# Optimization experiments

Measured on AMD Instinct MI355X. Metric: run time of the kernel, lower is better.

## Reference

```python
import jax, jax.numpy as jnp
import numpy as np

NUM_CLUSTERS = 5000  # labels.max()+1, fixed statically for jit
B, K, D, N = 256, 64, 2048, 50000
NHID, H2, NCLASS = 512, 256, 2


def setup_inputs() -> dict:
    key = jax.random.key(0)
    ks = jax.random.split(key, 16)
    s = lambda f_in: 1.0 / np.sqrt(f_in)
    return {
        "indexes": jax.random.randint(ks[0], (B,), 0, N),
        "features": jax.random.normal(ks[1], (N, D), dtype=jnp.float32),
        "labels": jax.random.randint(ks[2], (N,), 0, NUM_CLUSTERS),
        "domain": 1,
        "ori_0": 0,
        "ori_knn_neighbor": jax.random.randint(ks[3], (B, K), 0, N),
        "all_pred": jax.random.normal(ks[4], (B, K, NCLASS), dtype=jnp.float32),
        # GraphConv params (L-GCN style: weight [2*in, out])
        "W1": jax.random.normal(ks[5], (2 * D, NHID), jnp.float32) * s(2 * D),
        "b1": jnp.zeros((NHID,), jnp.float32),
        "W2": jax.random.normal(ks[6], (2 * NHID, H2), jnp.float32) * s(2 * NHID),
        "b2": jnp.zeros((H2,), jnp.float32),
        # classifier: Linear(256,256) -> PReLU(256) -> Linear(256,2)
        "Wc1": jax.random.normal(ks[7], (H2, H2), jnp.float32) * s(H2),
        "bc1": jnp.zeros((H2,), jnp.float32),
        "prelu_a": jnp.full((H2,), 0.25, jnp.float32),
        "Wc2": jax.random.normal(ks[8], (H2, NCLASS), jnp.float32) * s(H2),
        "bc2": jnp.zeros((NCLASS,), jnp.float32),
    }


def _gconv(x, A, W, b):
    # MeanAggregator: bmm(A, x); GraphConv: relu(cat([x, Ax]) @ W + b)
    agg = jnp.einsum('bkj,bjd->bkd', A, x)
    cat = jnp.concatenate([x, agg], axis=-1)
    return jax.nn.relu(jnp.einsum('bkd,df->bkf', cat, W) + b)


def reference(indexes, features, labels, domain, ori_0, ori_knn_neighbor, all_pred,
              W1, b1, W2, b2, Wc1, bc1, prelu_a, Wc2, bc2):
    # ---- cluster mean features (torch: index_add_ then divide; no_grad) ----
    clu_sum = jax.ops.segment_sum(features, labels, num_segments=NUM_CLUSTERS)
    nums = jax.ops.segment_sum(jnp.ones((features.shape[0],), features.dtype),
                               labels, num_segments=NUM_CLUSTERS)
    clu_mean = clu_sum / jnp.maximum(nums, 1.0)[:, None]  # [C, D]

    # ---- batched per-query subgraph construction (vectorized over B) ----
    clu_lab = labels[ori_knn_neighbor]            # [B, K]
    clu_feat = clu_mean[clu_lab]                  # [B, K, D]
    clu_feat = clu_feat.at[:, 0, :].set(features[indexes])  # pivot = raw feature

    A = jnp.einsum('bkd,bjd->bkj', clu_feat, clu_feat)       # pairwise similarity
    A = A * jnp.exp(all_pred[:, :, 1])[:, None, :]           # confidence weighting
    A = jax.nn.softmax(A, axis=-1)                           # row-normalized adjacency

    x = clu_feat / jnp.linalg.norm(clu_feat, axis=-1, keepdims=True)
    x = x - x[:, 0:1, :]                                     # center on pivot

    # (entire construction above is under torch.no_grad)
    x = jax.lax.stop_gradient(x)
    A = jax.lax.stop_gradient(A)

    # ---- GCN layers + classifier ----
    x = _gconv(x, A, W1, b1)      # [B, K, 512]
    x = _gconv(x, A, W2, b2)      # [B, K, 256]
    x0 = x.reshape(-1, H2)        # [B*K, 256]
    h = x0 @ Wc1 + bc1
    h = jnp.where(h >= 0, h, prelu_a * h)  # PReLU(256)
    logits = h @ Wc2 + bc2                 # [B*K, 2]

    # output_feat=True branch
    simm = jnp.sum(clu_mean * clu_mean, axis=1)                   # [C]
    pred = jax.nn.softmax(logits.reshape(B, K, NCLASS), axis=2)   # [B, K, 2]
    return (pred, simm)
```

## Files before the change

kernel.cpp:

```cpp
#include <hip/hip_runtime.h>
#include <math.h>

#define Bq 256
#define Kn 64
#define Dd 2048
#define Nn 50000
#define Cc 5000
#define NHID 512
#define H2d 256
#define LDH 264

typedef __attribute__((ext_vector_type(8))) __bf16 bf16x8;
typedef __attribute__((ext_vector_type(4))) float f32x4;

__device__ __forceinline__ unsigned short f2bf(float f) {
    union { float f; unsigned int u; } v;
    v.f = f;
    unsigned int u = v.u;
    unsigned int r = (u + 0x7fff + ((u >> 16) & 1)) >> 16;
    return (unsigned short)r;
}
__device__ __forceinline__ float bf2f(unsigned short h) {
    union { unsigned int u; float f; } v;
    v.u = ((unsigned int)h) << 16;
    return v.f;
}


__global__ void k_zero_int(int* __restrict__ p, int n) {
    int i = blockIdx.x * 256 + threadIdx.x;
    if (i < n) p[i] = 0;
}

__global__ void k_count(const int* __restrict__ labels, int* __restrict__ cnt, int n) {
    int i = blockIdx.x * 256 + threadIdx.x;
    if (i < n) atomicAdd(&cnt[labels[i]], 1);
}

__global__ __launch_bounds__(1024) void k_scan(const int* __restrict__ cnt,
                                               int* __restrict__ off,
                                               int* __restrict__ pos, int C) {
    __shared__ int s[1024];
    __shared__ int carry;
    int tid = threadIdx.x;
    if (tid == 0) carry = 0;
    __syncthreads();
    for (int base = 0; base < C; base += 1024) {
        int i = base + tid;
        int v = (i < C) ? cnt[i] : 0;
        s[tid] = v;
        __syncthreads();
        for (int o = 1; o < 1024; o <<= 1) {
            int t = (tid >= o) ? s[tid - o] : 0;
            __syncthreads();
            s[tid] += t;
            __syncthreads();
        }
        int excl = carry + s[tid] - v;
        if (i < C) { off[i] = excl; pos[i] = excl; }
        __syncthreads();
        if (tid == 0) carry += s[1023];
        __syncthreads();
    }
}

__global__ void k_scatter(const int* __restrict__ labels, int* __restrict__ pos,
                          int* __restrict__ rowidx, int n) {
    int i = blockIdx.x * 256 + threadIdx.x;
    if (i < n) {
        int p = atomicAdd(&pos[labels[i]], 1);
        rowidx[p] = i;
    }
}

__global__ __launch_bounds__(256) void k_meansimm(
    const float* __restrict__ feat, const int* __restrict__ rowidx,
    const int* __restrict__ off, const int* __restrict__ cnt,
    float* __restrict__ clu_mean, float* __restrict__ simm) {
    int c = blockIdx.x;
    int t = threadIdx.x;
    int n = cnt[c], st = off[c];
    float4 a0 = {0.f, 0.f, 0.f, 0.f}, a1 = {0.f, 0.f, 0.f, 0.f};
    for (int r = 0; r < n; r++) {
        const float* row = feat + (size_t)rowidx[st + r] * Dd;
        float4 v0 = *(const float4*)(row + t * 4);
        float4 v1 = *(const float4*)(row + 1024 + t * 4);
        a0.x += v0.x; a0.y += v0.y; a0.z += v0.z; a0.w += v0.w;
        a1.x += v1.x; a1.y += v1.y; a1.z += v1.z; a1.w += v1.w;
    }
    float sc = 1.f / (float)(n > 1 ? n : 1);
    a0.x *= sc; a0.y *= sc; a0.z *= sc; a0.w *= sc;
    a1.x *= sc; a1.y *= sc; a1.z *= sc; a1.w *= sc;
    float* outr = clu_mean + (size_t)c * Dd;
    *(float4*)(outr + t * 4) = a0;
    *(float4*)(outr + 1024 + t * 4) = a1;
    float ss = a0.x * a0.x + a0.y * a0.y + a0.z * a0.z + a0.w * a0.w +
               a1.x * a1.x + a1.y * a1.y + a1.z * a1.z + a1.w * a1.w;
    __shared__ float red[256];
    red[t] = ss;
    __syncthreads();
    for (int s2 = 128; s2 > 0; s2 >>= 1) {
        if (t < s2) red[t] += red[t + s2];
        __syncthreads();
    }
    if (t == 0) simm[c] = red[0];
}

__global__ __launch_bounds__(256) void k_build_ax(
    const float* __restrict__ feat, const float* __restrict__ clu_mean,
    const int* __restrict__ labels, const int* __restrict__ indexes,
    const int* __restrict__ knn, const float* __restrict__ all_pred,
    float* __restrict__ Abuf, unsigned short* __restrict__ xbuf) {
    __shared__ unsigned short Hs[64 * LDH];
    __shared__ unsigned short Ls[64 * LDH];
    __shared__ float Gs[64 * 65];
    __shared__ const float* rowp[64];
    __shared__ float wj64[64], rn[64];
    __shared__ float piv[2048];

    int b = blockIdx.x, tid = threadIdx.x;
    int wave = tid >> 6, lane = tid & 63, quad = lane >> 4, l16 = lane & 15;

    if (tid < 64) {
        const float* p = (tid == 0) ? feat + (size_t)indexes[b] * Dd
                                    : clu_mean + (size_t)labels[knn[b * 64 + tid]] * Dd;
        rowp[tid] = p;
        wj64[tid] = expf(all_pred[(b * 64 + tid) * 2 + 1]);
    }
    __syncthreads();

    f32x4 acc[4];
#pragma unroll
    for (int j = 0; j < 4; j++) acc[j] = (f32x4){0.f, 0.f, 0.f, 0.f};

    for (int ch = 0; ch < 8; ch++) {
        int d0 = ch * 256;
        __syncthreads();
#pragma unroll
        for (int q = 0; q < 16; q++) {
            int e4 = tid + q * 256;
            int row = e4 >> 6;
            int c4 = (e4 & 63) * 4;
            float4 v = *(const float4*)(rowp[row] + d0 + c4);
            ushort4 h, l;
            h.x = f2bf(v.x); l.x = f2bf(v.x - bf2f(h.x));
            h.y = f2bf(v.y); l.y = f2bf(v.y - bf2f(h.y));
            h.z = f2bf(v.z); l.z = f2bf(v.z - bf2f(h.z));
            h.w = f2bf(v.w); l.w = f2bf(v.w - bf2f(h.w));
            *(ushort4*)&Hs[row * LDH + c4] = h;
            *(ushort4*)&Ls[row * LDH + c4] = l;
        }
        __syncthreads();
#pragma unroll
        for (int ks = 0; ks < 8; ks++) {
            int kk = ks * 32 + quad * 8;
            bf16x8 ah = *(const bf16x8*)&Hs[(wave * 16 + l16) * LDH + kk];
            bf16x8 al = *(const bf16x8*)&Ls[(wave * 16 + l16) * LDH + kk];
#pragma unroll
            for (int j = 0; j < 4; j++) {
                bf16x8 bh = *(const bf16x8*)&Hs[(j * 16 + l16) * LDH + kk];
                bf16x8 bl = *(const bf16x8*)&Ls[(j * 16 + l16) * LDH + kk];
                acc[j] = __builtin_amdgcn_mfma_f32_16x16x32_bf16(ah, bh, acc[j], 0, 0, 0);
                acc[j] = __builtin_amdgcn_mfma_f32_16x16x32_bf16(ah, bl, acc[j], 0, 0, 0);
                acc[j] = __builtin_amdgcn_mfma_f32_16x16x32_bf16(al, bh, acc[j], 0, 0, 0);
            }
        }
    }
    __syncthreads();
#pragma unroll
    for (int j = 0; j < 4; j++)
#pragma unroll
        for (int r = 0; r < 4; r++)
            Gs[(wave * 16 + quad * 4 + r) * 65 + j * 16 + l16] = acc[j][r];
    __syncthreads();
    if (tid < 64) rn[tid] = rsqrtf(Gs[tid * 65 + tid]);
    __syncthreads();
    if (tid < 64) {
        int r = tid;
        float mx = -1e30f;
        for (int c = 0; c < 64; c++) {
            float v = Gs[r * 65 + c] * wj64[c];
            mx = fmaxf(mx, v);
        }
        float s = 0.f;
        for (int c = 0; c < 64; c++) {
            float e = expf(Gs[r * 65 + c] * wj64[c] - mx);
            Gs[r * 65 + c] = e;
            s += e;
        }
        float inv = 1.f / s;
        float* Arow = Abuf + ((size_t)b * 64 + r) * 64;
        for (int c = 0; c < 64; c++) Arow[c] = Gs[r * 65 + c] * inv;
    }
    __syncthreads();
    float rn0 = rn[0];
    const float* pivp = rowp[0];
    for (int c4 = tid; c4 < 512; c4 += 256) {
        float4 v = *(const float4*)(pivp + c4 * 4);
        v.x *= rn0; v.y *= rn0; v.z *= rn0; v.w *= rn0;
        *(float4*)&piv[c4 * 4] = v;
    }
    __syncthreads();
    unsigned short* xo = xbuf + (size_t)b * 64 * Dd;
    for (int e4 = tid; e4 < 64 * 512; e4 += 256) {
        int row = e4 >> 9;
        int c4 = (e4 & 511) * 4;
        float4 v = *(const float4*)(rowp[row] + c4);
        float r_ = rn[row];
        float4 p = *(const float4*)&piv[c4];
        ushort4 o_;
        o_.x = f2bf(v.x * r_ - p.x);
        o_.y = f2bf(v.y * r_ - p.y);
        o_.z = f2bf(v.z * r_ - p.z);
        o_.w = f2bf(v.w * r_ - p.w);
        *(ushort4*)&xo[row * Dd + c4] = o_;
    }
}

template <int SPLIT>
__global__ __launch_bounds__(256) void k_pack_w(const float* __restrict__ W,
                                                unsigned short* __restrict__ Bp,
                                                int K, int Nhalf) {
    int Ntot = SPLIT ? 2 * Nhalf : Nhalf;
    int idx = blockIdx.x * 256 + threadIdx.x;
    int kb = idx / Ntot;
    int n = idx - kb * Ntot;
    ushort4 lo, hi;
    float v[8];
#pragma unroll
    for (int j = 0; j < 8; j++) {
        int k = kb * 8 + j;
        if (SPLIT)
            v[j] = (n < Nhalf) ? W[(size_t)k * Nhalf + n]
                               : W[(size_t)(K + k) * Nhalf + (n - Nhalf)];
        else
            v[j] = W[(size_t)k * Nhalf + n];
    }
    lo.x = f2bf(v[0]); lo.y = f2bf(v[1]); lo.z = f2bf(v[2]); lo.w = f2bf(v[3]);
    hi.x = f2bf(v[4]); hi.y = f2bf(v[5]); hi.z = f2bf(v[6]); hi.w = f2bf(v[7]);
    *(ushort4*)&Bp[(size_t)idx * 8] = lo;
    *(ushort4*)&Bp[(size_t)idx * 8 + 4] = hi;
}

template <int EPI>
__global__ __launch_bounds__(256) void gemm_bf16_mfma(
    const unsigned short* __restrict__ A, const unsigned short* __restrict__ Bp,
    float* __restrict__ C, int M, int K, int N,
    const float* __restrict__ bias, const float* __restrict__ pre_a) {
    __shared__ unsigned short Asm[128 * 32];
    __shared__ unsigned short Bsm[4 * 128 * 8];
    int tid = threadIdx.x;
    int wave = tid >> 6, lane = tid & 63;
    int quad = lane >> 4, l16 = lane & 15;
    int m0 = blockIdx.y * 128, n0 = blockIdx.x * 128;
    int wm = (wave >> 1) * 64, wn = (wave & 1) * 64;

    f32x4 acc[4][4];
#pragma unroll
    for (int i = 0; i < 4; i++)
#pragma unroll
        for (int j = 0; j < 4; j++) acc[i][j] = (f32x4){0.f, 0.f, 0.f, 0.f};

    int ia0 = wave * 2, ia1 = wave * 2 + 1;
    const unsigned short* gA0 = A + (size_t)(m0 + ia0 * 16 + (lane >> 2)) * K + (lane & 3) * 8;
    const unsigned short* gA1 = gA0 + (size_t)16 * K;
    const unsigned short* gB0 = Bp + (size_t)(n0 + lane) * 8 + (size_t)wave * N * 8;

    for (int k0 = 0; k0 < K; k0 += 32) {
        __syncthreads();
        size_t bko = (size_t)(k0 >> 3) * N * 8;
        __builtin_amdgcn_global_load_lds(
            (const __attribute__((address_space(1))) void*)(gA0 + k0),
            (__attribute__((address_space(3))) void*)(Asm + ia0 * 512), 16, 0, 0);
        __builtin_amdgcn_global_load_lds(
            (const __attribute__((address_space(1))) void*)(gA1 + k0),
            (__attribute__((address_space(3))) void*)(Asm + ia1 * 512), 16, 0, 0);
        __builtin_amdgcn_global_load_lds(
            (const __attribute__((address_space(1))) void*)(gB0 + bko),
            (__attribute__((address_space(3))) void*)(Bsm + wave * 1024), 16, 0, 0);
        __builtin_amdgcn_global_load_lds(
            (const __attribute__((address_space(1))) void*)(gB0 + bko + 512),
            (__attribute__((address_space(3))) void*)(Bsm + wave * 1024 + 512), 16, 0, 0);
        __syncthreads();

        bf16x8 a[4], b[4];
#pragma unroll
        for (int i = 0; i < 4; i++)
            a[i] = *(const bf16x8*)&Asm[(wm + i * 16 + l16) * 32 + quad * 8];
#pragma unroll
        for (int j = 0; j < 4; j++)
            b[j] = *(const bf16x8*)&Bsm[quad * 1024 + (wn + j * 16 + l16) * 8];
#pragma unroll
        for (int i = 0; i < 4; i++)
#pragma unroll
            for (int j = 0; j < 4; j++)
                acc[i][j] = __builtin_amdgcn_mfma_f32_16x16x32_bf16(
                    a[i], b[j], acc[i][j], 0, 0, 0);
    }

#pragma unroll
    for (int i = 0; i < 4; i++) {
#pragma unroll
        for (int j = 0; j < 4; j++) {
            int col = n0 + wn + j * 16 + l16;
            float bcol = (EPI == 1) ? bias[col] : 0.f;
            float acol = (EPI == 1) ? pre_a[col] : 0.f;
#pragma unroll
            for (int r = 0; r < 4; r++) {
                int row = m0 + wm + i * 16 + quad * 4 + r;
                float v = acc[i][j][r];
                if (EPI == 1) {
                    v += bcol;
                    v = (v >= 0.f) ? v : acol * v;
                }
                C[(size_t)row * N + col] = v;
            }
        }
    }
}

template <int OBF>
__global__ __launch_bounds__(256) void k_layer_agg(
    const float* __restrict__ Uab, const float* __restrict__ Abuf,
    const float* __restrict__ bias, void* __restrict__ outp, int Nc) {
    int b = blockIdx.x;
    int tid = threadIdx.x;
    __shared__ float Ast[64 * 68];
    __shared__ float Us[64 * 68];
    int ty = tid >> 4, tx = tid & 15;
    const float* Ab = Abuf + (size_t)b * 64 * 64;
    for (int e4 = tid; e4 < 1024; e4 += 256) {
        float4 v = *(const float4*)(Ab + e4 * 4);
        int row = e4 >> 4;
        int c4 = (e4 & 15) * 4;
        Ast[(c4 + 0) * 68 + row] = v.x;
        Ast[(c4 + 1) * 68 + row] = v.y;
        Ast[(c4 + 2) * 68 + row] = v.z;
        Ast[(c4 + 3) * 68 + row] = v.w;
    }
    int ldU = 2 * Nc;
    const float* Ua = Uab;
    const float* Ub = Uab + Nc;
    for (int n0 = 0; n0 < Nc; n0 += 64) {
        __syncthreads();
#pragma unroll
        for (int kq = 0; kq < 4; kq++) {
            int e4 = tid + kq * 256;
            int row = e4 >> 4;
            int c4 = (e4 & 15) * 4;
            float4 v = *(const float4*)(Ub + (size_t)(b * 64 + row) * ldU + n0 + c4);
            *(float4*)&Us[row * 68 + c4] = v;
        }
        __syncthreads();
        float acc[4][4];
#pragma unroll
        for (int i = 0; i < 4; i++)
#pragma unroll
            for (int j = 0; j < 4; j++) acc[i][j] = 0.f;
        for (int kk = 0; kk < 64; kk++) {
            float4 a4 = *(const float4*)&Ast[kk * 68 + ty * 4];
            float4 b4 = *(const float4*)&Us[kk * 68 + tx * 4];
            float aa[4] = {a4.x, a4.y, a4.z, a4.w};
            float bb[4] = {b4.x, b4.y, b4.z, b4.w};
#pragma unroll
            for (int i = 0; i < 4; i++)
#pragma unroll
                for (int j = 0; j < 4; j++) acc[i][j] += aa[i] * bb[j];
        }
#pragma unroll
        for (int i = 0; i < 4; i++) {
            int m = b * 64 + ty * 4 + i;
            int n = n0 + tx * 4;
            float4 ua = *(const float4*)(Ua + (size_t)m * ldU + n);
            float v0 = fmaxf(ua.x + acc[i][0] + bias[n + 0], 0.f);
            float v1 = fmaxf(ua.y + acc[i][1] + bias[n + 1], 0.f);
            float v2 = fmaxf(ua.z + acc[i][2] + bias[n + 2], 0.f);
            float v3 = fmaxf(ua.w + acc[i][3] + bias[n + 3], 0.f);
            if (OBF) {
                ushort4 o_;
                o_.x = f2bf(v0); o_.y = f2bf(v1); o_.z = f2bf(v2); o_.w = f2bf(v3);
                *(ushort4*)((unsigned short*)outp + (size_t)m * Nc + n) = o_;
            } else {
                float4 o_ = {v0, v1, v2, v3};
                *(float4*)((float*)outp + (size_t)m * Nc + n) = o_;
            }
        }
        __syncthreads();
    }
}

__global__ __launch_bounds__(256) void k_logits(
    const float* __restrict__ h, const float* __restrict__ Wc2,
    const float* __restrict__ bc2, float* __restrict__ pred) {
    __shared__ float p0[256], p1[256];
    int tid = threadIdx.x;
    int r = tid >> 2, s = tid & 3;
    int m = blockIdx.x * 64 + r;
    const float* hr = h + (size_t)m * 256;
    float l0 = 0.f, l1 = 0.f;
    for (int k = s; k < 256; k += 4) {
        float hv = hr[k];
        l0 += hv * Wc2[2 * k];
        l1 += hv * Wc2[2 * k + 1];
    }
    p0[tid] = l0;
    p1[tid] = l1;
    __syncthreads();
    if (s == 0) {
        float L0 = p0[tid] + p0[tid + 1] + p0[tid + 2] + p0[tid + 3] + bc2[0];
        float L1 = p1[tid] + p1[tid + 1] + p1[tid + 2] + p1[tid + 3] + bc2[1];
        float mx = fmaxf(L0, L1);
        float e0 = expf(L0 - mx), e1 = expf(L1 - mx);
        float inv = 1.f / (e0 + e1);
        pred[2 * m] = e0 * inv;
        pred[2 * m + 1] = e1 * inv;
    }
}

extern "C" void kernel_launch(void* const* d_in, const int* in_sizes, int n_in,
                              void* d_out, int out_size, void* d_ws, size_t ws_size,
                              hipStream_t stream) {
    const int* indexes = (const int*)d_in[0];
    const float* features = (const float*)d_in[1];
    const int* labels = (const int*)d_in[2];
    const int* knn = (const int*)d_in[5];
    const float* all_pred = (const float*)d_in[6];
    const float* W1 = (const float*)d_in[7];
    const float* b1 = (const float*)d_in[8];
    const float* W2 = (const float*)d_in[9];
    const float* b2 = (const float*)d_in[10];
    const float* Wc1 = (const float*)d_in[11];
    const float* bc1 = (const float*)d_in[12];
    const float* pre_a = (const float*)d_in[13];
    const float* Wc2 = (const float*)d_in[14];
    const float* bc2 = (const float*)d_in[15];
    float* out = (float*)d_out;

    char* w = (char*)d_ws;
    size_t o = 0;
    auto carve = [&](size_t bytes) -> char* {
        char* p = w + o;
        o += (bytes + 255) & ~(size_t)255;
        return p;
    };
    int* cnt = (int*)carve((size_t)Cc * 4);
    int* off = (int*)carve((size_t)Cc * 4);
    int* pos = (int*)carve((size_t)Cc * 4);
    int* rowidx = (int*)carve((size_t)Nn * 4);
    float* clu_mean = (float*)carve((size_t)Cc * Dd * 4);
    unsigned short* xbuf = (unsigned short*)carve((size_t)Bq * Kn * Dd * 2);
    float* Abuf = (float*)carve((size_t)Bq * Kn * Kn * 4);
    float* U = (float*)carve((size_t)Bq * Kn * 2 * NHID * 4);
    unsigned short* Bp1 = (unsigned short*)carve((size_t)(Dd / 8) * 1024 * 8 * 2);
    unsigned short* x1 = (unsigned short*)carve((size_t)Bq * Kn * NHID * 2);
    float* V = (float*)carve((size_t)Bq * Kn * 2 * H2d * 4);
    unsigned short* Bp2 = (unsigned short*)carve((size_t)(NHID / 8) * 512 * 8 * 2);
    unsigned short* x2 = (unsigned short*)carve((size_t)Bq * Kn * H2d * 2);
    float* h = (float*)carve((size_t)Bq * Kn * H2d * 4);
    unsigned short* Bpc = (unsigned short*)carve((size_t)(H2d / 8) * 256 * 8 * 2);

    float* simm_out = out + (size_t)Bq * Kn * 2;

    k_zero_int<<<(Cc + 255) / 256, 256, 0, stream>>>(cnt, Cc);
    k_count<<<(Nn + 255) / 256, 256, 0, stream>>>(labels, cnt, Nn);
    k_scan<<<1, 1024, 0, stream>>>(cnt, off, pos, Cc);
    k_scatter<<<(Nn + 255) / 256, 256, 0, stream>>>(labels, pos, rowidx, Nn);

    k_meansimm<<<Cc, 256, 0, stream>>>(features, rowidx, off, cnt, clu_mean, simm_out);

    k_build_ax<<<Bq, 256, 0, stream>>>(features, clu_mean, labels, indexes, knn,
                                       all_pred, Abuf, xbuf);

    k_pack_w<1><<<(Dd / 8) * 1024 / 256, 256, 0, stream>>>(W1, Bp1, Dd, NHID);
    k_pack_w<1><<<(NHID / 8) * 512 / 256, 256, 0, stream>>>(W2, Bp2, NHID, H2d);
    k_pack_w<0><<<(H2d / 8) * 256 / 256, 256, 0, stream>>>(Wc1, Bpc, H2d, H2d);

    {
        dim3 g(1024 / 128, (Bq * Kn) / 128);
        gemm_bf16_mfma<0><<<g, 256, 0, stream>>>(xbuf, Bp1, U, Bq * Kn, Dd, 1024,
                                                 nullptr, nullptr);
    }
    k_layer_agg<1><<<Bq, 256, 0, stream>>>(U, Abuf, b1, x1, NHID);

    {
        dim3 g(512 / 128, (Bq * Kn) / 128);
        gemm_bf16_mfma<0><<<g, 256, 0, stream>>>(x1, Bp2, V, Bq * Kn, NHID, 512,
                                                 nullptr, nullptr);
    }
    k_layer_agg<1><<<Bq, 256, 0, stream>>>(V, Abuf, b2, x2, H2d);

    {
        dim3 g(256 / 128, (Bq * Kn) / 128);
        gemm_bf16_mfma<1><<<g, 256, 0, stream>>>(x2, Bpc, h, Bq * Kn, H2d, 256,
                                                 bc1, pre_a);
    }
    k_logits<<<(Bq * Kn) / 64, 256, 0, stream>>>(h, Wc2, bc2, out);

    (void)in_sizes; (void)n_in; (void)out_size; (void)ws_size;
}
```

Before: 906.7 us.

## Project unique cluster means through W1 once instead of per-neighbor rows

The first GCN layer's input rows are now built from a table of normalized cluster means plus normalized pivot rows (5376 rows in total). The first projection GEMM runs on that table instead of on 16384 materialized B*K rows, and the subtraction of the pivot is moved after the projection by linearity. A new aggregation kernel gathers the projected rows by label and subtracts the pivot's projection before the A-aggregation and ReLU. This removes the 64MB xbuf write and cuts the big GEMM's M dimension roughly threefold. In exchange it adds a pivot kernel, a padding zero-fill, gathered reads in the aggregation, and a slightly different rounding order (bf16 applied before the subtraction).

Measured after the change: 837.4 us. 1.08x faster.

```diff
diff --git a/kernel.cpp b/kernel.cpp
--- a/kernel.cpp
+++ b/kernel.cpp
@@ -9,6 +9,8 @@
 #define NHID 512
 #define H2d 256
 #define LDH 264
+#define MP 5376
+#define PIVROW 5120
 
 typedef __attribute__((ext_vector_type(8))) __bf16 bf16x8;
 typedef __attribute__((ext_vector_type(4))) float f32x4;
@@ -76,7 +78,8 @@
 __global__ __launch_bounds__(256) void k_meansimm(
     const float* __restrict__ feat, const int* __restrict__ rowidx,
     const int* __restrict__ off, const int* __restrict__ cnt,
-    float* __restrict__ clu_mean, float* __restrict__ simm) {
+    float* __restrict__ clu_mean, float* __restrict__ simm,
+    unsigned short* __restrict__ cn) {
     int c = blockIdx.x;
     int t = threadIdx.x;
     int n = cnt[c], st = off[c];
@@ -104,19 +107,56 @@
         __syncthreads();
     }
     if (t == 0) simm[c] = red[0];
+    float tot = red[0];
+    float rnn = (tot > 0.f) ? rsqrtf(tot) : 0.f;
+    ushort4 c0, c1;
+    c0.x = f2bf(a0.x * rnn); c0.y = f2bf(a0.y * rnn);
+    c0.z = f2bf(a0.z * rnn); c0.w = f2bf(a0.w * rnn);
+    c1.x = f2bf(a1.x * rnn); c1.y = f2bf(a1.y * rnn);
+    c1.z = f2bf(a1.z * rnn); c1.w = f2bf(a1.w * rnn);
+    unsigned short* cr = cn + (size_t)c * Dd;
+    *(ushort4*)(cr + t * 4) = c0;
+    *(ushort4*)(cr + 1024 + t * 4) = c1;
+}
+
+__global__ __launch_bounds__(256) void k_pivots(
+    const float* __restrict__ feat, const int* __restrict__ indexes,
+    unsigned short* __restrict__ PA) {
+    int b = blockIdx.x, t = threadIdx.x;
+    const float* row = feat + (size_t)indexes[b] * Dd;
+    float4 v0 = *(const float4*)(row + t * 4);
+    float4 v1 = *(const float4*)(row + 1024 + t * 4);
+    float ss = v0.x * v0.x + v0.y * v0.y + v0.z * v0.z + v0.w * v0.w +
+               v1.x * v1.x + v1.y * v1.y + v1.z * v1.z + v1.w * v1.w;
+    __shared__ float red[256];
+    red[t] = ss;
+    __syncthreads();
+    for (int s2 = 128; s2 > 0; s2 >>= 1) {
+        if (t < s2) red[t] += red[t + s2];
+        __syncthreads();
+    }
+    float tot = red[0];
+    float rnn = (tot > 0.f) ? rsqrtf(tot) : 0.f;
+    ushort4 c0, c1;
+    c0.x = f2bf(v0.x * rnn); c0.y = f2bf(v0.y * rnn);
+    c0.z = f2bf(v0.z * rnn); c0.w = f2bf(v0.w * rnn);
+    c1.x = f2bf(v1.x * rnn); c1.y = f2bf(v1.y * rnn);
+    c1.z = f2bf(v1.z * rnn); c1.w = f2bf(v1.w * rnn);
+    unsigned short* cr = PA + (size_t)(PIVROW + b) * Dd;
+    *(ushort4*)(cr + t * 4) = c0;
+    *(ushort4*)(cr + 1024 + t * 4) = c1;
 }
 
 __global__ __launch_bounds__(256) void k_build_ax(
     const float* __restrict__ feat, const float* __restrict__ clu_mean,
     const int* __restrict__ labels, const int* __restrict__ indexes,
     const int* __restrict__ knn, const float* __restrict__ all_pred,
-    float* __restrict__ Abuf, unsigned short* __restrict__ xbuf) {
+    float* __restrict__ Abuf) {
     __shared__ unsigned short Hs[64 * LDH];
     __shared__ unsigned short Ls[64 * LDH];
     __shared__ float Gs[64 * 65];
     __shared__ const float* rowp[64];
-    __shared__ float wj64[64], rn[64];
-    __shared__ float piv[2048];
+    __shared__ float wj64[64];
 
     int b = blockIdx.x, tid = threadIdx.x;
     int wave = tid >> 6, lane = tid & 63, quad = lane >> 4, l16 = lane & 15;
@@ -173,8 +213,6 @@
         for (int r = 0; r < 4; r++)
             Gs[(wave * 16 + quad * 4 + r) * 65 + j * 16 + l16] = acc[j][r];
     __syncthreads();
-    if (tid < 64) rn[tid] = rsqrtf(Gs[tid * 65 + tid]);
-    __syncthreads();
     if (tid < 64) {
         int r = tid;
         float mx = -1e30f;
@@ -191,29 +229,6 @@
         float inv = 1.f / s;
         float* Arow = Abuf + ((size_t)b * 64 + r) * 64;
         for (int c = 0; c < 64; c++) Arow[c] = Gs[r * 65 + c] * inv;
-    }
-    __syncthreads();
-    float rn0 = rn[0];
-    const float* pivp = rowp[0];
-    for (int c4 = tid; c4 < 512; c4 += 256) {
-        float4 v = *(const float4*)(pivp + c4 * 4);
-        v.x *= rn0; v.y *= rn0; v.z *= rn0; v.w *= rn0;
-        *(float4*)&piv[c4 * 4] = v;
-    }
-    __syncthreads();
-    unsigned short* xo = xbuf + (size_t)b * 64 * Dd;
-    for (int e4 = tid; e4 < 64 * 512; e4 += 256) {
-        int row = e4 >> 9;
-        int c4 = (e4 & 511) * 4;
-        float4 v = *(const float4*)(rowp[row] + c4);
-        float r_ = rn[row];
-        float4 p = *(const float4*)&piv[c4];
-        ushort4 o_;
-        o_.x = f2bf(v.x * r_ - p.x);
-        o_.y = f2bf(v.y * r_ - p.y);
-        o_.z = f2bf(v.z * r_ - p.z);
-        o_.w = f2bf(v.w * r_ - p.w);
-        *(ushort4*)&xo[row * Dd + c4] = o_;
     }
 }
 
@@ -316,6 +331,76 @@
                 C[(size_t)row * N + col] = v;
             }
         }
+    }
+}
+
+__global__ __launch_bounds__(256) void k_layer_agg1(
+    const float* __restrict__ P, const float* __restrict__ Abuf,
+    const int* __restrict__ labels, const int* __restrict__ knn,
+    const float* __restrict__ bias, unsigned short* __restrict__ outp) {
+    int b = blockIdx.x;
+    int tid = threadIdx.x;
+    __shared__ float Ast[64 * 68];
+    __shared__ float Us[64 * 68];
+    __shared__ int rowid[64];
+    int ty = tid >> 4, tx = tid & 15;
+    if (tid < 64)
+        rowid[tid] = (tid == 0) ? (PIVROW + b) : labels[knn[b * 64 + tid]];
+    const float* Ab = Abuf + (size_t)b * 64 * 64;
+    for (int e4 = tid; e4 < 1024; e4 += 256) {
+        float4 v = *(const float4*)(Ab + e4 * 4);
+        int row = e4 >> 4;
+        int c4 = (e4 & 15) * 4;
+        Ast[(c4 + 0) * 68 + row] = v.x;
+        Ast[(c4 + 1) * 68 + row] = v.y;
+        Ast[(c4 + 2) * 68 + row] = v.z;
+        Ast[(c4 + 3) * 68 + row] = v.w;
+    }
+    const float* Q = P + (size_t)(PIVROW + b) * 1024;
+    for (int n0 = 0; n0 < NHID; n0 += 64) {
+        __syncthreads();
+#pragma unroll
+        for (int kq = 0; kq < 4; kq++) {
+            int e4 = tid + kq * 256;
+            int row = e4 >> 4;
+            int c4 = (e4 & 15) * 4;
+            float4 v = *(const float4*)(P + (size_t)rowid[row] * 1024 + NHID + n0 + c4);
+            float4 q = *(const float4*)(Q + NHID + n0 + c4);
+            v.x -= q.x; v.y -= q.y; v.z -= q.z; v.w -= q.w;
+            *(float4*)&Us[row * 68 + c4] = v;
+        }
+        __syncthreads();
+        float acc[4][4];
+#pragma unroll
+        for (int i = 0; i < 4; i++)
+#pragma unroll
+            for (int j = 0; j < 4; j++) acc[i][j] = 0.f;
+        for (int kk = 0; kk < 64; kk++) {
+            float4 a4 = *(const float4*)&Ast[kk * 68 + ty * 4];
+            float4 b4 = *(const float4*)&Us[kk * 68 + tx * 4];
+            float aa[4] = {a4.x, a4.y, a4.z, a4.w};
+            float bb[4] = {b4.x, b4.y, b4.z, b4.w};
+#pragma unroll
+            for (int i = 0; i < 4; i++)
+#pragma unroll
+                for (int j = 0; j < 4; j++) acc[i][j] += aa[i] * bb[j];
+        }
+#pragma unroll
+        for (int i = 0; i < 4; i++) {
+            int krow = ty * 4 + i;
+            int m = b * 64 + krow;
+            int n = n0 + tx * 4;
+            float4 ua = *(const float4*)(P + (size_t)rowid[krow] * 1024 + n);
+            float4 qa = *(const float4*)(Q + n);
+            float v0 = fmaxf(ua.x - qa.x + acc[i][0] + bias[n + 0], 0.f);
+            float v1 = fmaxf(ua.y - qa.y + acc[i][1] + bias[n + 1], 0.f);
+            float v2 = fmaxf(ua.z - qa.z + acc[i][2] + bias[n + 2], 0.f);
+            float v3 = fmaxf(ua.w - qa.w + acc[i][3] + bias[n + 3], 0.f);
+            ushort4 o_;
+            o_.x = f2bf(v0); o_.y = f2bf(v1); o_.z = f2bf(v2); o_.w = f2bf(v3);
+            *(ushort4*)(outp + (size_t)m * NHID + n) = o_;
+        }
+        __syncthreads();
     }
 }
 
@@ -448,9 +533,9 @@
     int* pos = (int*)carve((size_t)Cc * 4);
     int* rowidx = (int*)carve((size_t)Nn * 4);
     float* clu_mean = (float*)carve((size_t)Cc * Dd * 4);
-    unsigned short* xbuf = (unsigned short*)carve((size_t)Bq * Kn * Dd * 2);
+    unsigned short* PA = (unsigned short*)carve((size_t)MP * Dd * 2);
+    float* Pout = (float*)carve((size_t)MP * 2 * NHID * 4);
     float* Abuf = (float*)carve((size_t)Bq * Kn * Kn * 4);
-    float* U = (float*)carve((size_t)Bq * Kn * 2 * NHID * 4);
     unsigned short* Bp1 = (unsigned short*)carve((size_t)(Dd / 8) * 1024 * 8 * 2);
     unsigned short* x1 = (unsigned short*)carve((size_t)Bq * Kn * NHID * 2);
     float* V = (float*)carve((size_t)Bq * Kn * 2 * H2d * 4);
@@ -466,21 +551,30 @@
     k_scan<<<1, 1024, 0, stream>>>(cnt, off, pos, Cc);
     k_scatter<<<(Nn + 255) / 256, 256, 0, stream>>>(labels, pos, rowidx, Nn);
 
-    k_meansimm<<<Cc, 256, 0, stream>>>(features, rowidx, off, cnt, clu_mean, simm_out);
+    {
+        int npad = (PIVROW - Cc) * Dd / 2;
+        k_zero_int<<<(npad + 255) / 256, 256, 0, stream>>>(
+            (int*)(PA + (size_t)Cc * Dd), npad);
+    }
+
+    k_meansimm<<<Cc, 256, 0, stream>>>(features, rowidx, off, cnt, clu_mean,
+                                       simm_out, PA);
+
+    k_pivots<<<Bq, 256, 0, stream>>>(features, indexes, PA);
 
     k_build_ax<<<Bq, 256, 0, stream>>>(features, clu_mean, labels, indexes, knn,
-                                       all_pred, Abuf, xbuf);
+                                       all_pred, Abuf);
 
     k_pack_w<1><<<(Dd / 8) * 1024 / 256, 256, 0, stream>>>(W1, Bp1, Dd, NHID);
     k_pack_w<1><<<(NHID / 8) * 512 / 256, 256, 0, stream>>>(W2, Bp2, NHID, H2d);
     k_pack_w<0><<<(H2d / 8) * 256 / 256, 256, 0, stream>>>(Wc1, Bpc, H2d, H2d);
 
     {
-        dim3 g(1024 / 128, (Bq * Kn) / 128);
-        gemm_bf16_mfma<0><<<g, 256, 0, stream>>>(xbuf, Bp1, U, Bq * Kn, Dd, 1024,
+        dim3 g(1024 / 128, MP / 128);
+        gemm_bf16_mfma<0><<<g, 256, 0, stream>>>(PA, Bp1, Pout, MP, Dd, 1024,
                                                  nullptr, nullptr);
     }
-    k_layer_agg<1><<<Bq, 256, 0, stream>>>(U, Abuf, b1, x1, NHID);
+    k_layer_agg1<<<Bq, 256, 0, stream>>>(Pout, Abuf, labels, knn, b1, x1);
 
     {
         dim3 g(512 / 128, (Bq * Kn) / 128);
```
